# Kernel optimization log

Measured on AMD Instinct MI355X. Metric: run time of the kernel, lower is better.

Reference implementation:

```python
import jax, jax.numpy as jnp
import numpy as np

HEADS = 8
EPS = 1e-5


def _layernorm(x, g, b):
    mu = jnp.mean(x, axis=-1, keepdims=True)
    var = jnp.mean(jnp.square(x - mu), axis=-1, keepdims=True)
    return (x - mu) * jax.lax.rsqrt(var + EPS) * g + b


def setup_inputs() -> dict:
    key = jax.random.key(0)
    ks = jax.random.split(key, 10)
    B, S, D = 4, 2048, 256
    d_ff = 2 * D
    s = 0.02
    return {
        "x": jax.random.normal(ks[0], (B, S, D), dtype=jnp.float32),
        "ln1_g": jnp.ones((D,), jnp.float32),
        "ln1_b": jnp.zeros((D,), jnp.float32),
        "w_qkv": jax.random.normal(ks[1], (3 * D, D), jnp.float32) * s,
        "b_qkv": jnp.zeros((3 * D,), jnp.float32),
        "w_proj": jax.random.normal(ks[2], (D, D), jnp.float32) * s,
        "b_proj": jnp.zeros((D,), jnp.float32),
        "ln2_g": jnp.ones((D,), jnp.float32),
        "ln2_b": jnp.zeros((D,), jnp.float32),
        "w1": jax.random.normal(ks[3], (d_ff, D), jnp.float32) * s,
        "b1": jnp.zeros((d_ff,), jnp.float32),
        "w2": jax.random.normal(ks[4], (D, d_ff), jnp.float32) * s,
        "b2": jnp.zeros((D,), jnp.float32),
    }


def reference(x, ln1_g, ln1_b, w_qkv, b_qkv, w_proj, b_proj,
              ln2_g, ln2_b, w1, b1, w2, b2):
    B, S, D = x.shape
    H = HEADS
    dh = D // H
    scale = dh ** -0.5

    # --- attention sublayer (pre-LN) ---
    y = _layernorm(x, ln1_g, ln1_b)
    qkv = y @ w_qkv.T + b_qkv                       # [B,S,3D]
    qkv = qkv.reshape(B, S, 3, H, dh)
    q = jnp.transpose(qkv[:, :, 0], (0, 2, 1, 3))   # [B,H,S,dh]
    k = jnp.transpose(qkv[:, :, 1], (0, 2, 1, 3))
    v = jnp.transpose(qkv[:, :, 2], (0, 2, 1, 3))
    attn = jax.nn.softmax(jnp.einsum('bhsd,bhtd->bhst', q, k) * scale, axis=-1)
    ctx = jnp.einsum('bhst,bhtd->bhsd', attn, v)    # [B,H,S,dh]
    ctx = jnp.transpose(ctx, (0, 2, 1, 3)).reshape(B, S, D)
    x = x + ctx @ w_proj.T + b_proj

    # --- FFN sublayer (pre-LN) ---
    y = _layernorm(x, ln2_g, ln2_b)
    h = jax.nn.silu(y @ w1.T + b1)                  # [B,S,2D]
    x = x + h @ w2.T + b2
    return x
```

## Files before the change

### kernel.cpp

```cpp
#include <hip/hip_runtime.h>
#include <cstddef>

constexpr int kB   = 4;
constexpr int kS   = 2048;
constexpr int kD   = 256;
constexpr int kH   = 8;
constexpr int kDH  = 32;
constexpr int kDFF = 512;
constexpr int kM   = kB * kS;
constexpr float kEps = 1e-5f;
constexpr float kScaleL2E = 0.17677669529663687f * 1.4426950408889634f;

typedef float f32x4  __attribute__((ext_vector_type(4)));
typedef short bf16x8 __attribute__((ext_vector_type(8)));
typedef unsigned short u16;
typedef unsigned int   u32;

__device__ inline u16 f2bf(float x) {
    union { float f; unsigned u; } c; c.f = x;
    const unsigned r = c.u + 0x7fffu + ((c.u >> 16) & 1u);
    return (u16)(r >> 16);
}

__device__ inline u32 pk_trunc(float lo, float hi) {
    union { float f; u32 u; } a, b; a.f = lo; b.f = hi;
    return __builtin_amdgcn_perm(b.u, a.u, 0x07060302u);
}

__global__ __launch_bounds__(256)
void ln_kernel(const float* __restrict__ x, const float* __restrict__ g,
               const float* __restrict__ b, u16* __restrict__ y)
{
    const int wave = threadIdx.x >> 6;
    const int lane = threadIdx.x & 63;
    const int row  = blockIdx.x * 4 + wave;
    const float4 v = *(const float4*)&x[(size_t)row * kD + lane * 4];
    float s1 = (v.x + v.y) + (v.z + v.w);
    float s2 = (v.x * v.x + v.y * v.y) + (v.z * v.z + v.w * v.w);
    #pragma unroll
    for (int off = 1; off < 64; off <<= 1) {
        s1 += __shfl_xor(s1, off);
        s2 += __shfl_xor(s2, off);
    }
    const float mu  = s1 * (1.0f / kD);
    const float var = s2 * (1.0f / kD) - mu * mu;
    const float inv = rsqrtf(var + kEps);
    const float4 g4 = *(const float4*)&g[lane * 4];
    const float4 b4 = *(const float4*)&b[lane * 4];
    *(ushort4*)&y[(size_t)row * kD + lane * 4] = make_ushort4(
        f2bf((v.x - mu) * inv * g4.x + b4.x),
        f2bf((v.y - mu) * inv * g4.y + b4.y),
        f2bf((v.z - mu) * inv * g4.z + b4.z),
        f2bf((v.w - mu) * inv * g4.w + b4.w));
}

template<int NT, int OUTMODE, bool RES, int KTOT>
__global__ __launch_bounds__(256)
void gemm_bf16(const u16* __restrict__ A, const float* __restrict__ Wf,
               const float* __restrict__ bias, const float* __restrict__ res,
               float* __restrict__ Cf, u16* __restrict__ Cb,
               u16* __restrict__ KbP, u16* __restrict__ VtP, int N)
{
    constexpr int BSTR = KTOT + 4;
    __shared__ u16 Bs[NT * BSTR];
    const int tid  = threadIdx.x;
    const int wave = tid >> 6;
    const int lane = tid & 63;
    const int quad = lane >> 4;
    const int l16  = lane & 15;
    const int m0 = blockIdx.x * 64;
    const int n0 = blockIdx.y * NT;

    {
        constexpr int ITS = (NT * KTOT) / 1024;
        #pragma unroll
        for (int it = 0; it < ITS; ++it) {
            const int e   = it * 1024 + tid * 4;
            const int row = e / KTOT;
            const int col = e & (KTOT - 1);
            const float4 wv = *(const float4*)&Wf[(size_t)(n0 + row) * KTOT + col];
            *(ushort4*)&Bs[row * BSTR + col] = make_ushort4(
                f2bf(wv.x), f2bf(wv.y), f2bf(wv.z), f2bf(wv.w));
        }
    }
    __syncthreads();

    f32x4 acc[NT / 16];
    #pragma unroll
    for (int ni = 0; ni < NT / 16; ++ni) acc[ni] = {0.f, 0.f, 0.f, 0.f};

    const u16* arow = &A[(size_t)(m0 + wave * 16 + l16) * KTOT];
    #pragma unroll 4
    for (int k0 = 0; k0 < KTOT; k0 += 32) {
        const bf16x8 a = *(const bf16x8*)&arow[k0 + quad * 8];
        #pragma unroll
        for (int ni = 0; ni < NT / 16; ++ni) {
            const bf16x8 bf = *(const bf16x8*)&Bs[(ni * 16 + l16) * BSTR + k0 + quad * 8];
            acc[ni] = __builtin_amdgcn_mfma_f32_16x16x32_bf16(a, bf, acc[ni], 0, 0, 0);
        }
    }

    #pragma unroll
    for (int ni = 0; ni < NT / 16; ++ni) {
        const float bias_v = bias[n0 + ni * 16 + l16];
        #pragma unroll
        for (int r = 0; r < 4; ++r) {
            const int m = m0 + wave * 16 + quad * 4 + r;
            float v = acc[ni][r] + bias_v;
            if (OUTMODE == 0) {
                const int n = n0 + ni * 16 + l16;
                if (RES) v += res[(size_t)m * N + n];
                Cf[(size_t)m * N + n] = v;
            } else if (OUTMODE == 1) {
                const int n = n0 + ni * 16 + l16;
                v = v / (1.0f + __expf(-v));
                Cb[(size_t)m * N + n] = f2bf(v);
            } else {
                const int rgn = n0 >> 8;
                const int nl  = (n0 & 255) + ni * 16 + l16;
                const int hh  = nl >> 5, dh = nl & 31;
                const int bb  = m >> 11, s = m & (kS - 1);
                const int bh  = bb * kH + hh;
                if (rgn == 0)
                    Cb[((size_t)bh * kS + s) * kDH + dh] = f2bf(v * kScaleL2E);
                else if (rgn == 1)
                    KbP[((size_t)bh * kS + s) * kDH + dh] = f2bf(v);
                else {
                    const int so = s & 127;
                    const int p  = ((so & 15) << 3) | (so >> 4);
                    VtP[((size_t)bh * (kS / 128) + (s >> 7)) * 4096
                        + (p >> 3) * 256 + dh * 8 + (p & 7)] = f2bf(v);
                }
            }
        }
    }
}

constexpr int kPStrU = 136;

__global__ __launch_bounds__(256)
void attn_kernel(const u16* __restrict__ Qb, const u16* __restrict__ Kb,
                 const u16* __restrict__ Vp, u16* __restrict__ ctx)
{
    __shared__ __align__(16) u16 pbuf[4][32 * kPStrU];
    const int tid  = threadIdx.x;
    const int wave = tid >> 6;
    const int lane = tid & 63;
    const int quad = lane >> 4;
    const int l16  = lane & 15;
    const int h = blockIdx.y;
    const int b = blockIdx.z;
    const int bh = b * kH + h;
    const int qsub = wave >> 1;
    const int half = wave & 1;
    const int q0 = blockIdx.x * 64 + qsub * 32;

    bf16x8 aq[2];
    aq[0] = *(const bf16x8*)&Qb[((size_t)bh * kS + q0 + l16) * kDH + quad * 8];
    aq[1] = *(const bf16x8*)&Qb[((size_t)bh * kS + q0 + 16 + l16) * kDH + quad * 8];

    const u16* Kbase = Kb + (size_t)bh * kS * kDH;
    const u16* Vbase = Vp + (size_t)bh * kS * kDH;
    u16* pw = pbuf[wave];

    f32x4 O[2][2] = {};
    f32x4 lp[2] = {};
    const f32x4 zz = {0.f, 0.f, 0.f, 0.f};

    const int kbeg = half * (kS / 2);
    #pragma unroll 1
    for (int kt = kbeg; kt < kbeg + kS / 2; kt += 128) {
        bf16x8 kf[8];
        #pragma unroll
        for (int kg = 0; kg < 8; ++kg)
            kf[kg] = *(const bf16x8*)
                &Kbase[(size_t)(kt + kg * 16 + l16) * kDH + quad * 8];
        const u16* vtile = Vbase + (size_t)(kt >> 7) * 4096;
        bf16x8 vf[4][2];
        #pragma unroll
        for (int ks = 0; ks < 2; ++ks)
            #pragma unroll
            for (int nf = 0; nf < 2; ++nf)
                vf[ks][nf] = *(const bf16x8*)
                    &vtile[(ks * 4 + quad) * 256 + (nf * 16 + l16) * 8];

        #pragma unroll
        for (int qb = 0; qb < 2; ++qb) {
            f32x4 S[8];
            #pragma unroll
            for (int kg = 0; kg < 8; ++kg)
                S[kg] = __builtin_amdgcn_mfma_f32_16x16x32_bf16(aq[qb], kf[kg], zz, 0, 0, 0);
            #pragma unroll
            for (int r = 0; r < 4; ++r) {
                float e[8];
                #pragma unroll
                for (int kg = 0; kg < 8; ++kg) e[kg] = exp2f(S[kg][r]);
                lp[qb][r] += ((e[0] + e[1]) + (e[2] + e[3]))
                           + ((e[4] + e[5]) + (e[6] + e[7]));
                uint4 pk;
                pk.x = pk_trunc(e[0], e[1]);
                pk.y = pk_trunc(e[2], e[3]);
                pk.z = pk_trunc(e[4], e[5]);
                pk.w = pk_trunc(e[6], e[7]);
                *(uint4*)&pw[(qb * 16 + quad * 4 + r) * kPStrU + l16 * 8] = pk;
            }
        }

        #pragma unroll
        for (int ks = 2; ks < 4; ++ks)
            #pragma unroll
            for (int nf = 0; nf < 2; ++nf)
                vf[ks][nf] = *(const bf16x8*)
                    &vtile[(ks * 4 + quad) * 256 + (nf * 16 + l16) * 8];

        #pragma unroll
        for (int qb = 0; qb < 2; ++qb)
            #pragma unroll
            for (int ks = 0; ks < 4; ++ks) {
                const bf16x8 pA = *(const bf16x8*)
                    &pw[(qb * 16 + l16) * kPStrU + ks * 32 + quad * 8];
                O[qb][0] = __builtin_amdgcn_mfma_f32_16x16x32_bf16(pA, vf[ks][0], O[qb][0], 0, 0, 0);
                O[qb][1] = __builtin_amdgcn_mfma_f32_16x16x32_bf16(pA, vf[ks][1], O[qb][1], 0, 0, 0);
            }
    }

    #pragma unroll
    for (int off = 1; off < 16; off <<= 1)
        #pragma unroll
        for (int qb = 0; qb < 2; ++qb)
            #pragma unroll
            for (int r = 0; r < 4; ++r)
                lp[qb][r] += __shfl_xor(lp[qb][r], off);

    __syncthreads();
    float* cb = (float*)&pbuf[0][0] + qsub * (32 * 33);
    if (half == 1) {
        #pragma unroll
        for (int qb = 0; qb < 2; ++qb)
            #pragma unroll
            for (int r = 0; r < 4; ++r) {
                const int row = qb * 16 + quad * 4 + r;
                cb[row * 33 + l16]      = O[qb][0][r];
                cb[row * 33 + 16 + l16] = O[qb][1][r];
                if (l16 == 0) cb[row * 33 + 32] = lp[qb][r];
            }
    }
    __syncthreads();
    if (half == 0) {
        #pragma unroll
        for (int qb = 0; qb < 2; ++qb)
            #pragma unroll
            for (int r = 0; r < 4; ++r) {
                const int row = qb * 16 + quad * 4 + r;
                const float l   = lp[qb][r] + cb[row * 33 + 32];
                const float inv = 1.0f / l;
                const float o0 = O[qb][0][r] + cb[row * 33 + l16];
                const float o1 = O[qb][1][r] + cb[row * 33 + 16 + l16];
                const int q = q0 + row;
                u16* crow = ctx + ((size_t)(b * kS + q)) * kD + h * kDH;
                crow[l16]      = f2bf(o0 * inv);
                crow[16 + l16] = f2bf(o1 * inv);
            }
    }
}

extern "C" void kernel_launch(void* const* d_in, const int* in_sizes, int n_in,
                              void* d_out, int out_size, void* d_ws, size_t ws_size,
                              hipStream_t stream)
{
    const float* x      = (const float*)d_in[0];
    const float* ln1_g  = (const float*)d_in[1];
    const float* ln1_b  = (const float*)d_in[2];
    const float* w_qkv  = (const float*)d_in[3];
    const float* b_qkv  = (const float*)d_in[4];
    const float* w_proj = (const float*)d_in[5];
    const float* b_proj = (const float*)d_in[6];
    const float* ln2_g  = (const float*)d_in[7];
    const float* ln2_b  = (const float*)d_in[8];
    const float* w1     = (const float*)d_in[9];
    const float* b1     = (const float*)d_in[10];
    const float* w2     = (const float*)d_in[11];
    const float* b2     = (const float*)d_in[12];
    float* out = (float*)d_out;

    char* ws = (char*)d_ws;
    u16* Qb  = (u16*)ws;
    u16* Kb  = (u16*)(ws + ((size_t)4  << 20));
    u16* Vp  = (u16*)(ws + ((size_t)8  << 20));
    u16* ctx = (u16*)(ws + ((size_t)12 << 20));
    u16* y   = (u16*)(ws + ((size_t)16 << 20));
    u16* h   = (u16*)ws;

    const dim3 blk(256);

    ln_kernel<<<dim3(kM / 4), blk, 0, stream>>>(x, ln1_g, ln1_b, y);
    gemm_bf16<64, 2, false, 256><<<dim3(kM / 64, 12), blk, 0, stream>>>(
        y, w_qkv, b_qkv, nullptr, nullptr, Qb, Kb, Vp, 0);
    attn_kernel<<<dim3(kS / 64, kH, kB), blk, 0, stream>>>(Qb, Kb, Vp, ctx);
    gemm_bf16<32, 0, true, 256><<<dim3(kM / 64, kD / 32), blk, 0, stream>>>(
        ctx, w_proj, b_proj, x, out, nullptr, nullptr, nullptr, kD);
    ln_kernel<<<dim3(kM / 4), blk, 0, stream>>>(out, ln2_g, ln2_b, y);
    gemm_bf16<64, 1, false, 256><<<dim3(kM / 64, kDFF / 64), blk, 0, stream>>>(
        y, w1, b1, nullptr, nullptr, h, nullptr, nullptr, kDFF);
    gemm_bf16<32, 0, true, 512><<<dim3(kM / 64, kD / 32), blk, 0, stream>>>(
        h, w2, b2, out, out, nullptr, nullptr, nullptr, kD);
}
```

Measured before the change: 188.7 us.

## Split attention keys across four waves and loop GEMM blocks over two M tiles

The attention kernel now gives each block 32 queries and splits the key range four ways across its waves, processing 64-key tiles. The V permutation layout changes to match, and the partial outputs from all four waves are reduced through shared memory. Each GEMM block now computes two 64-row M tiles, so the weight tile is converted into LDS once per two tiles and the grid is halved. The aim is more attention blocks in flight and less repeated weight staging, at the cost of extra cross-wave reduction work and fewer, longer GEMM blocks.

```diff
diff --git a/kernel.cpp b/kernel.cpp
--- a/kernel.cpp
+++ b/kernel.cpp
@@ -54,7 +54,7 @@
         f2bf((v.w - mu) * inv * g4.w + b4.w));
 }
 
-template<int NT, int OUTMODE, bool RES, int KTOT>
+template<int NT, int OUTMODE, bool RES, int KTOT, int MLOOP>
 __global__ __launch_bounds__(256)
 void gemm_bf16(const u16* __restrict__ A, const float* __restrict__ Wf,
                const float* __restrict__ bias, const float* __restrict__ res,
@@ -68,7 +68,7 @@
     const int lane = tid & 63;
     const int quad = lane >> 4;
     const int l16  = lane & 15;
-    const int m0 = blockIdx.x * 64;
+    const int mbase = blockIdx.x * (64 * MLOOP);
     const int n0 = blockIdx.y * NT;
 
     {
@@ -85,58 +85,61 @@
     }
     __syncthreads();
 
-    f32x4 acc[NT / 16];
-    #pragma unroll
-    for (int ni = 0; ni < NT / 16; ++ni) acc[ni] = {0.f, 0.f, 0.f, 0.f};
-
-    const u16* arow = &A[(size_t)(m0 + wave * 16 + l16) * KTOT];
-    #pragma unroll 4
-    for (int k0 = 0; k0 < KTOT; k0 += 32) {
-        const bf16x8 a = *(const bf16x8*)&arow[k0 + quad * 8];
+    #pragma unroll 1
+    for (int mi = 0; mi < MLOOP; ++mi) {
+        const int m0 = mbase + mi * 64;
+
+        f32x4 acc[NT / 16];
+        #pragma unroll
+        for (int ni = 0; ni < NT / 16; ++ni) acc[ni] = {0.f, 0.f, 0.f, 0.f};
+
+        const u16* arow = &A[(size_t)(m0 + wave * 16 + l16) * KTOT];
+        #pragma unroll 4
+        for (int k0 = 0; k0 < KTOT; k0 += 32) {
+            const bf16x8 a = *(const bf16x8*)&arow[k0 + quad * 8];
+            #pragma unroll
+            for (int ni = 0; ni < NT / 16; ++ni) {
+                const bf16x8 bf = *(const bf16x8*)&Bs[(ni * 16 + l16) * BSTR + k0 + quad * 8];
+                acc[ni] = __builtin_amdgcn_mfma_f32_16x16x32_bf16(a, bf, acc[ni], 0, 0, 0);
+            }
+        }
+
         #pragma unroll
         for (int ni = 0; ni < NT / 16; ++ni) {
-            const bf16x8 bf = *(const bf16x8*)&Bs[(ni * 16 + l16) * BSTR + k0 + quad * 8];
-            acc[ni] = __builtin_amdgcn_mfma_f32_16x16x32_bf16(a, bf, acc[ni], 0, 0, 0);
+            const float bias_v = bias[n0 + ni * 16 + l16];
+            #pragma unroll
+            for (int r = 0; r < 4; ++r) {
+                const int m = m0 + wave * 16 + quad * 4 + r;
+                float v = acc[ni][r] + bias_v;
+                if (OUTMODE == 0) {
+                    const int n = n0 + ni * 16 + l16;
+                    if (RES) v += res[(size_t)m * N + n];
+                    Cf[(size_t)m * N + n] = v;
+                } else if (OUTMODE == 1) {
+                    const int n = n0 + ni * 16 + l16;
+                    v = v / (1.0f + __expf(-v));
+                    Cb[(size_t)m * N + n] = f2bf(v);
+                } else {
+                    const int rgn = n0 >> 8;
+                    const int nl  = (n0 & 255) + ni * 16 + l16;
+                    const int hh  = nl >> 5, dh = nl & 31;
+                    const int bb  = m >> 11, s = m & (kS - 1);
+                    const int bh  = bb * kH + hh;
+                    if (rgn == 0)
+                        Cb[((size_t)bh * kS + s) * kDH + dh] = f2bf(v * kScaleL2E);
+                    else if (rgn == 1)
+                        KbP[((size_t)bh * kS + s) * kDH + dh] = f2bf(v);
+                    else {
+                        const int sp = (s & ~63) | (((s & 15) << 2) | ((s >> 4) & 3));
+                        VtP[(((size_t)bh * (kS / 8) + (sp >> 3)) * kDH + dh) * 8 + (sp & 7)] = f2bf(v);
+                    }
+                }
+            }
         }
     }
-
-    #pragma unroll
-    for (int ni = 0; ni < NT / 16; ++ni) {
-        const float bias_v = bias[n0 + ni * 16 + l16];
-        #pragma unroll
-        for (int r = 0; r < 4; ++r) {
-            const int m = m0 + wave * 16 + quad * 4 + r;
-            float v = acc[ni][r] + bias_v;
-            if (OUTMODE == 0) {
-                const int n = n0 + ni * 16 + l16;
-                if (RES) v += res[(size_t)m * N + n];
-                Cf[(size_t)m * N + n] = v;
-            } else if (OUTMODE == 1) {
-                const int n = n0 + ni * 16 + l16;
-                v = v / (1.0f + __expf(-v));
-                Cb[(size_t)m * N + n] = f2bf(v);
-            } else {
-                const int rgn = n0 >> 8;
-                const int nl  = (n0 & 255) + ni * 16 + l16;
-                const int hh  = nl >> 5, dh = nl & 31;
-                const int bb  = m >> 11, s = m & (kS - 1);
-                const int bh  = bb * kH + hh;
-                if (rgn == 0)
-                    Cb[((size_t)bh * kS + s) * kDH + dh] = f2bf(v * kScaleL2E);
-                else if (rgn == 1)
-                    KbP[((size_t)bh * kS + s) * kDH + dh] = f2bf(v);
-                else {
-                    const int so = s & 127;
-                    const int p  = ((so & 15) << 3) | (so >> 4);
-                    VtP[((size_t)bh * (kS / 128) + (s >> 7)) * 4096
-                        + (p >> 3) * 256 + dh * 8 + (p & 7)] = f2bf(v);
-                }
-            }
-        }
-    }
-}
-
-constexpr int kPStrU = 136;
+}
+
+constexpr int kPStrU = 72;
 
 __global__ __launch_bounds__(256)
 void attn_kernel(const u16* __restrict__ Qb, const u16* __restrict__ Kb,
@@ -151,9 +154,7 @@
     const int h = blockIdx.y;
     const int b = blockIdx.z;
     const int bh = b * kH + h;
-    const int qsub = wave >> 1;
-    const int half = wave & 1;
-    const int q0 = blockIdx.x * 64 + qsub * 32;
+    const int q0 = blockIdx.x * 32;
 
     bf16x8 aq[2];
     aq[0] = *(const bf16x8*)&Qb[((size_t)bh * kS + q0 + l16) * kDH + quad * 8];
@@ -167,56 +168,47 @@
     f32x4 lp[2] = {};
     const f32x4 zz = {0.f, 0.f, 0.f, 0.f};
 
-    const int kbeg = half * (kS / 2);
+    const int kbeg = wave * (kS / 4);
     #pragma unroll 1
-    for (int kt = kbeg; kt < kbeg + kS / 2; kt += 128) {
-        bf16x8 kf[8];
-        #pragma unroll
-        for (int kg = 0; kg < 8; ++kg)
+    for (int kt = kbeg; kt < kbeg + kS / 4; kt += 64) {
+        bf16x8 kf[4];
+        #pragma unroll
+        for (int kg = 0; kg < 4; ++kg)
             kf[kg] = *(const bf16x8*)
                 &Kbase[(size_t)(kt + kg * 16 + l16) * kDH + quad * 8];
-        const u16* vtile = Vbase + (size_t)(kt >> 7) * 4096;
-        bf16x8 vf[4][2];
+        bf16x8 vf[2][2];
         #pragma unroll
         for (int ks = 0; ks < 2; ++ks)
             #pragma unroll
             for (int nf = 0; nf < 2; ++nf)
                 vf[ks][nf] = *(const bf16x8*)
-                    &vtile[(ks * 4 + quad) * 256 + (nf * 16 + l16) * 8];
+                    &Vbase[(size_t)((((kt + ks * 32 + quad * 8) >> 3) * kDH
+                                     + nf * 16 + l16) << 3)];
 
         #pragma unroll
         for (int qb = 0; qb < 2; ++qb) {
-            f32x4 S[8];
-            #pragma unroll
-            for (int kg = 0; kg < 8; ++kg)
+            f32x4 S[4];
+            #pragma unroll
+            for (int kg = 0; kg < 4; ++kg)
                 S[kg] = __builtin_amdgcn_mfma_f32_16x16x32_bf16(aq[qb], kf[kg], zz, 0, 0, 0);
             #pragma unroll
             for (int r = 0; r < 4; ++r) {
-                float e[8];
-                #pragma unroll
-                for (int kg = 0; kg < 8; ++kg) e[kg] = exp2f(S[kg][r]);
-                lp[qb][r] += ((e[0] + e[1]) + (e[2] + e[3]))
-                           + ((e[4] + e[5]) + (e[6] + e[7]));
-                uint4 pk;
-                pk.x = pk_trunc(e[0], e[1]);
-                pk.y = pk_trunc(e[2], e[3]);
-                pk.z = pk_trunc(e[4], e[5]);
-                pk.w = pk_trunc(e[6], e[7]);
-                *(uint4*)&pw[(qb * 16 + quad * 4 + r) * kPStrU + l16 * 8] = pk;
+                const float e0 = exp2f(S[0][r]);
+                const float e1 = exp2f(S[1][r]);
+                const float e2 = exp2f(S[2][r]);
+                const float e3 = exp2f(S[3][r]);
+                lp[qb][r] += (e0 + e1) + (e2 + e3);
+                uint2 pk;
+                pk.x = pk_trunc(e0, e1);
+                pk.y = pk_trunc(e2, e3);
+                *(uint2*)&pw[(qb * 16 + quad * 4 + r) * kPStrU + l16 * 4] = pk;
             }
         }
 
         #pragma unroll
-        for (int ks = 2; ks < 4; ++ks)
-            #pragma unroll
-            for (int nf = 0; nf < 2; ++nf)
-                vf[ks][nf] = *(const bf16x8*)
-                    &vtile[(ks * 4 + quad) * 256 + (nf * 16 + l16) * 8];
-
-        #pragma unroll
         for (int qb = 0; qb < 2; ++qb)
             #pragma unroll
-            for (int ks = 0; ks < 4; ++ks) {
+            for (int ks = 0; ks < 2; ++ks) {
                 const bf16x8 pA = *(const bf16x8*)
                     &pw[(qb * 16 + l16) * kPStrU + ks * 32 + quad * 8];
                 O[qb][0] = __builtin_amdgcn_mfma_f32_16x16x32_bf16(pA, vf[ks][0], O[qb][0], 0, 0, 0);
@@ -233,8 +225,9 @@
                 lp[qb][r] += __shfl_xor(lp[qb][r], off);
 
     __syncthreads();
-    float* cb = (float*)&pbuf[0][0] + qsub * (32 * 33);
-    if (half == 1) {
+    float* cbase = (float*)&pbuf[0][0];
+    if (wave > 0) {
+        float* cb = cbase + (wave - 1) * (32 * 33);
         #pragma unroll
         for (int qb = 0; qb < 2; ++qb)
             #pragma unroll
@@ -246,16 +239,23 @@
             }
     }
     __syncthreads();
-    if (half == 0) {
+    if (wave == 0) {
         #pragma unroll
         for (int qb = 0; qb < 2; ++qb)
             #pragma unroll
             for (int r = 0; r < 4; ++r) {
                 const int row = qb * 16 + quad * 4 + r;
-                const float l   = lp[qb][r] + cb[row * 33 + 32];
+                float l  = lp[qb][r];
+                float o0 = O[qb][0][r];
+                float o1 = O[qb][1][r];
+                #pragma unroll
+                for (int s = 0; s < 3; ++s) {
+                    const float* cb = cbase + s * (32 * 33);
+                    o0 += cb[row * 33 + l16];
+                    o1 += cb[row * 33 + 16 + l16];
+                    l  += cb[row * 33 + 32];
+                }
                 const float inv = 1.0f / l;
-                const float o0 = O[qb][0][r] + cb[row * 33 + l16];
-                const float o1 = O[qb][1][r] + cb[row * 33 + 16 + l16];
                 const int q = q0 + row;
                 u16* crow = ctx + ((size_t)(b * kS + q)) * kD + h * kDH;
                 crow[l16]      = f2bf(o0 * inv);
@@ -294,14 +294,14 @@
     const dim3 blk(256);
 
     ln_kernel<<<dim3(kM / 4), blk, 0, stream>>>(x, ln1_g, ln1_b, y);
-    gemm_bf16<64, 2, false, 256><<<dim3(kM / 64, 12), blk, 0, stream>>>(
+    gemm_bf16<64, 2, false, 256, 2><<<dim3(kM / 128, 12), blk, 0, stream>>>(
         y, w_qkv, b_qkv, nullptr, nullptr, Qb, Kb, Vp, 0);
-    attn_kernel<<<dim3(kS / 64, kH, kB), blk, 0, stream>>>(Qb, Kb, Vp, ctx);
-    gemm_bf16<32, 0, true, 256><<<dim3(kM / 64, kD / 32), blk, 0, stream>>>(
+    attn_kernel<<<dim3(kS / 32, kH, kB), blk, 0, stream>>>(Qb, Kb, Vp, ctx);
+    gemm_bf16<32, 0, true, 256, 2><<<dim3(kM / 128, kD / 32), blk, 0, stream>>>(
         ctx, w_proj, b_proj, x, out, nullptr, nullptr, nullptr, kD);
     ln_kernel<<<dim3(kM / 4), blk, 0, stream>>>(out, ln2_g, ln2_b, y);
-    gemm_bf16<64, 1, false, 256><<<dim3(kM / 64, kDFF / 64), blk, 0, stream>>>(
+    gemm_bf16<64, 1, false, 256, 2><<<dim3(kM / 128, kDFF / 64), blk, 0, stream>>>(
         y, w1, b1, nullptr, nullptr, h, nullptr, nullptr, kDFF);
-    gemm_bf16<32, 0, true, 512><<<dim3(kM / 64, kD / 32), blk, 0, stream>>>(
+    gemm_bf16<32, 0, true, 512, 2><<<dim3(kM / 128, kD / 32), blk, 0, stream>>>(
         h, w2, b2, out, out, nullptr, nullptr, nullptr, kD);
 }
```

Result: faster. 184.6 us (-2.2%).
